# Performance work log

Measured on AMD Instinct MI355X. Metric: run time of the kernel, lower is better.

The kernel has to match this reference:

```python
import jax, jax.numpy as jnp
import numpy as np

B, T, D = 4, 2048, 1024
H, DK, DV = 16, 64, 64


def setup_inputs() -> dict:
    key = jax.random.key(0)
    ks = jax.random.split(key, 12)
    std = 1.0 / np.sqrt(D)
    inp = {
        "query": jax.random.normal(ks[0], (B, T, D), jnp.float32),
        "key": jax.random.normal(ks[1], (B, T, D), jnp.float32),
        "value": jax.random.normal(ks[2], (B, T, D), jnp.float32),
        "mask": jnp.ones((B, 1, 1, T), dtype=bool),
        # weights stored as [in, out] (torch Linear applies x @ W.T + b)
        "Wq": jax.random.truncated_normal(ks[3], -2, 2, (D, H * DK), jnp.float32) * std,
        "bq": jnp.zeros((H * DK,), jnp.float32),
        "Wk": jax.random.truncated_normal(ks[4], -2, 2, (D, H * DK), jnp.float32) * std,
        "bk": jnp.zeros((H * DK,), jnp.float32),
        "Wv": jax.random.truncated_normal(ks[5], -2, 2, (D, H * DV), jnp.float32) * std,
        "bv": jnp.zeros((H * DV,), jnp.float32),
        "Wo": jax.random.truncated_normal(ks[6], -2, 2, (H * DV, D), jnp.float32) * (1.0 / np.sqrt(H * DV)),
        "bo": jnp.zeros((D,), jnp.float32),
    }
    return inp


def reference(query, key, value, mask, Wq, bq, Wk, bk, Wv, bv, Wo, bo):
    denom = 1.0 / np.sqrt(DK)
    q = (query @ Wq + bq).reshape(B, T, H, DK)
    k = (key @ Wk + bk).reshape(B, T, H, DK)
    v = (value @ Wv + bv).reshape(B, T, H, DV)
    # [B, H, T, T] attention logits
    logits = jnp.einsum("bthd,bThd->bhtT", q, k) * denom
    logits = jnp.where(mask, logits, -1e30)
    w = jax.nn.softmax(logits, axis=-1)
    attn = jnp.einsum("bhtT,bThd->bthd", w, v).reshape(B, T, H * DV)
    return attn @ Wo + bo
```

## Files before the change

kernel.cpp:

```cpp
#include <hip/hip_runtime.h>


typedef _Float16 f16;
typedef f16 f16x4 __attribute__((ext_vector_type(4)));
typedef f16 f16x8 __attribute__((ext_vector_type(8)));
typedef __fp16 h16x2 __attribute__((ext_vector_type(2)));
typedef float f32x4 __attribute__((ext_vector_type(4)));

__device__ __forceinline__ void gload_lds16(const void* g, void* l) {
  __builtin_amdgcn_global_load_lds(
      (const __attribute__((address_space(1))) unsigned int*)g,
      (__attribute__((address_space(3))) unsigned int*)l, 16, 0, 0);
}

__device__ __forceinline__ f16x8 cvt8(const f32x4& a, const f32x4& b) {
  h16x2 r0 = __builtin_amdgcn_cvt_pkrtz(a[0], a[1]);
  h16x2 r1 = __builtin_amdgcn_cvt_pkrtz(a[2], a[3]);
  h16x2 r2 = __builtin_amdgcn_cvt_pkrtz(b[0], b[1]);
  h16x2 r3 = __builtin_amdgcn_cvt_pkrtz(b[2], b[3]);
  f16x8 w;
  w[0] = (f16)r0[0]; w[1] = (f16)r0[1]; w[2] = (f16)r1[0]; w[3] = (f16)r1[1];
  w[4] = (f16)r2[0]; w[5] = (f16)r2[1]; w[6] = (f16)r3[0]; w[7] = (f16)r3[1];
  return w;
}

__global__ __launch_bounds__(256) void wtrans(const float* __restrict__ W,
                                              f16* __restrict__ WT) {
  __shared__ float tile[32][33];
  int tx = threadIdx.x, ty = threadIdx.y;
  int o0 = blockIdx.x * 32, i0 = blockIdx.y * 32;
#pragma unroll
  for (int r = 0; r < 32; r += 8)
    tile[ty + r][tx] = W[(size_t)(i0 + ty + r) * 1024 + o0 + tx];
  __syncthreads();
#pragma unroll
  for (int r = 0; r < 32; r += 8)
    WT[(size_t)(o0 + ty + r) * 1024 + i0 + tx] = (f16)tile[tx][ty + r];
}

template <int MODE, bool AF32>
__global__ __launch_bounds__(256) void gemm_bt(const void* __restrict__ Av,
                                               const f16* __restrict__ Bt,
                                               const float* __restrict__ bias,
                                               f16* __restrict__ C16,
                                               float* __restrict__ C32) {
  constexpr int N = 1024, K = 1024;
  constexpr int BM = 128, BN = 128, BK = 32;
  __shared__ f16 As[BM * BK];
  __shared__ f16 Bs[BN * BK];

  const int t = threadIdx.x;
  const int nb = gridDim.x;
  int bid = blockIdx.x;
  int cpx = nb >> 3;
  int swz = (bid & 7) * cpx + (bid >> 3);
  const int ntile = N / BN;
  const int tm = swz / ntile, tn = swz % ntile;

  const int lane = t & 63, w = t >> 6;
  const int wr = w >> 1, wc = w & 1;
  const int lrow = lane & 15, kgrp = lane >> 4;

  f32x4 zero4 = {0.f, 0.f, 0.f, 0.f};
  f32x4 acc[4][4];
#pragma unroll
  for (int mi = 0; mi < 4; ++mi)
#pragma unroll
    for (int ni = 0; ni < 4; ++ni) acc[mi][ni] = zero4;

  const int srow = t >> 2;
  const int scol = (t & 3) * 8;
  const f16* Ag = (const f16*)Av + (size_t)(tm * BM + srow) * K + scol;
  const float* Ag32 = (const float*)Av + (size_t)(tm * BM + srow) * K + scol;
  const f16* Bg = Bt + (size_t)(tn * BN + srow) * K + scol;
  f16* Asl = &As[t * 8];
  f16* Bsl = &Bs[t * 8];

  f32x4 ar[4];
  auto loadA = [&](int k0) {
    ar[0] = *(const f32x4*)(Ag32 + k0);
    ar[1] = *(const f32x4*)(Ag32 + k0 + 4);
    ar[2] = *(const f32x4*)(Ag32 + (size_t)64 * K + k0);
    ar[3] = *(const f32x4*)(Ag32 + (size_t)64 * K + k0 + 4);
  };

  if (AF32) loadA(0);
  for (int k0 = 0; k0 < K; k0 += BK) {
    __syncthreads();
    if (AF32) {
      *(f16x8*)Asl = cvt8(ar[0], ar[1]);
      *(f16x8*)(Asl + 64 * BK) = cvt8(ar[2], ar[3]);
    } else {
      gload_lds16(Ag + k0, Asl);
      gload_lds16(Ag + k0 + (size_t)64 * K, Asl + 64 * BK);
    }
    gload_lds16(Bg + k0, Bsl);
    gload_lds16(Bg + k0 + (size_t)64 * K, Bsl + 64 * BK);
    __syncthreads();
    if (AF32 && k0 + BK < K) loadA(k0 + BK);

    f16x8 af[4], bf[4];
#pragma unroll
    for (int mi = 0; mi < 4; ++mi)
      af[mi] = *(const f16x8*)&As[(wr * 64 + mi * 16 + lrow) * BK + kgrp * 8];
#pragma unroll
    for (int ni = 0; ni < 4; ++ni)
      bf[ni] = *(const f16x8*)&Bs[(wc * 64 + ni * 16 + lrow) * BK + kgrp * 8];
#pragma unroll
    for (int mi = 0; mi < 4; ++mi)
#pragma unroll
      for (int ni = 0; ni < 4; ++ni)
        acc[mi][ni] = __builtin_amdgcn_mfma_f32_16x16x32_f16(af[mi], bf[ni],
                                                             acc[mi][ni], 0, 0, 0);
  }

#pragma unroll
  for (int mi = 0; mi < 4; ++mi) {
#pragma unroll
    for (int ni = 0; ni < 4; ++ni) {
      int col = tn * BN + wc * 64 + ni * 16 + lrow;
      float bv = bias[col];
#pragma unroll
      for (int j = 0; j < 4; ++j) {
        int row = tm * BM + wr * 64 + mi * 16 + kgrp * 4 + j;
        float v = acc[mi][ni][j] + bv;
        if (MODE == 0) {
          C16[(size_t)row * N + col] = (f16)v;
        } else if (MODE == 1) {
          int bb = row >> 11, tt = row & 2047;
          C16[((size_t)(bb * 1024 + col)) * 2048 + tt] = (f16)v;
        } else {
          C32[(size_t)row * N + col] = v;
        }
      }
    }
  }
}

__global__ __launch_bounds__(256) void attn_fwd(const f16* __restrict__ Q,
                                                const f16* __restrict__ Kc,
                                                const f16* __restrict__ Vt,
                                                f16* __restrict__ O) {
  constexpr int T = 2048, HD = 1024, KLD = 88;
  __shared__ f16 Ks[64 * KLD];
  __shared__ f16 Vs[64 * 64];

  const int t = threadIdx.x;
  const int lane = t & 63, w = t >> 6;
  const int lrow = lane & 15, kgrp = lane >> 4;
  int bid = blockIdx.x;
  int swzb = (bid & 7) * 128 + (bid >> 3);
  const int qt = swzb & 15, h = (swzb >> 4) & 15, b = swzb >> 8;

  f16x8 aq[2][2];
#pragma unroll
  for (int g = 0; g < 2; ++g) {
    const f16* qp = Q + (size_t)(b * T + qt * 128 + w * 32 + g * 16 + lrow) * HD +
                    h * 64 + kgrp * 8;
    aq[g][0] = (*(const f16x8*)(qp)) * (f16)0.18033688f;
    aq[g][1] = (*(const f16x8*)(qp + 32)) * (f16)0.18033688f;
  }

  f32x4 zero4 = {0.f, 0.f, 0.f, 0.f};
  float m_r[2] = {-INFINITY, -INFINITY}, l_r[2] = {0.f, 0.f};
  f32x4 oa0[4], oa1[4];
#pragma unroll
  for (int d = 0; d < 4; ++d) { oa0[d] = zero4; oa1[d] = zero4; }

  const int srow = t >> 3;
  const int scol = (t & 7) * 8;
  const int vblk = (t & 7) * 2;
  const int vswz = ((srow & 7) << 1) | ((srow >> 3) & 1);
  const int rswz = ((lrow & 7) << 1) | (lrow >> 3);
  const f16* Kg = Kc + (size_t)(b * T + srow) * HD + h * 64 + scol;
  const f16* Vg = Vt + (size_t)(b * 1024 + h * 64 + srow) * T + scol;

  f16x8 ka0, ka1, va0, va1, kb0, kb1, vb0, vb1;

  auto load_a = [&](int kt) {
    ka0 = *(const f16x8*)(Kg + (size_t)kt * HD);
    ka1 = *(const f16x8*)(Kg + (size_t)(kt + 32) * HD);
    va0 = *(const f16x8*)(Vg + kt);
    va1 = *(const f16x8*)(Vg + kt + 32 * T);
  };
  auto load_b = [&](int kt) {
    kb0 = *(const f16x8*)(Kg + (size_t)kt * HD);
    kb1 = *(const f16x8*)(Kg + (size_t)(kt + 32) * HD);
    vb0 = *(const f16x8*)(Vg + kt);
    vb1 = *(const f16x8*)(Vg + kt + 32 * T);
  };
  auto store_set = [&](f16x8& k0, f16x8& k1, f16x8& v0, f16x8& v1) {
    *(f16x8*)&Ks[srow * KLD + scol] = k0;
    *(f16x8*)&Ks[(srow + 32) * KLD + scol] = k1;
    f16x4* v0h = (f16x4*)&v0;
    f16x4* v1h = (f16x4*)&v1;
    *(f16x4*)&Vs[srow * 64 + ((vblk) ^ vswz) * 4] = v0h[0];
    *(f16x4*)&Vs[srow * 64 + ((vblk + 1) ^ vswz) * 4] = v0h[1];
    *(f16x4*)&Vs[(srow + 32) * 64 + ((vblk) ^ vswz) * 4] = v1h[0];
    *(f16x4*)&Vs[(srow + 32) * 64 + ((vblk + 1) ^ vswz) * 4] = v1h[1];
  };

  auto softmax = [&](f32x4* s, float& mr, float& lr, f32x4* oacc, f16x4* pa) {
    float m0 = fmaxf(fmaxf(s[0][0], s[0][1]), s[0][2]);
    float m1 = fmaxf(fmaxf(s[0][3], s[1][0]), s[1][1]);
    float m2 = fmaxf(fmaxf(s[1][2], s[1][3]), s[2][0]);
    float m3 = fmaxf(fmaxf(s[2][1], s[2][2]), s[2][3]);
    float m4 = fmaxf(fmaxf(s[3][0], s[3][1]), s[3][2]);
    float mx = fmaxf(fmaxf(fmaxf(m0, m1), m2), fmaxf(fmaxf(m3, m4), s[3][3]));
    mx = fmaxf(mx, __shfl_xor(mx, 16, 64));
    mx = fmaxf(mx, __shfl_xor(mx, 32, 64));
    if (__any(mx > mr + 8.f)) {
      float mnew = fmaxf(mr, mx);
      float sc = exp2f(mr - mnew);
      lr *= sc;
      mr = mnew;
#pragma unroll
      for (int d = 0; d < 4; ++d) {
        f32x4 t4 = oacc[d];
        t4[0] *= sc; t4[1] *= sc; t4[2] *= sc; t4[3] *= sc;
        oacc[d] = t4;
      }
    }
    float rs = 0.f;
#pragma unroll
    for (int n = 0; n < 4; ++n) {
      f32x4 p;
#pragma unroll
      for (int j = 0; j < 4; ++j) {
        p[j] = exp2f(s[n][j] - mr);
        rs += p[j];
      }
      h16x2 lo = __builtin_amdgcn_cvt_pkrtz(p[0], p[1]);
      h16x2 hi = __builtin_amdgcn_cvt_pkrtz(p[2], p[3]);
      f16x4 q4;
      q4[0] = (f16)lo[0]; q4[1] = (f16)lo[1];
      q4[2] = (f16)hi[0]; q4[3] = (f16)hi[1];
      pa[n] = q4;
    }
    rs += __shfl_xor(rs, 16, 64);
    rs += __shfl_xor(rs, 32, 64);
    lr += rs;
  };

  auto compute = [&]() {
    f16x8 kf[4][2];
#pragma unroll
    for (int n = 0; n < 4; ++n)
#pragma unroll
      for (int kk = 0; kk < 2; ++kk)
        kf[n][kk] = *(const f16x8*)&Ks[(n * 16 + lrow) * KLD + kk * 32 + kgrp * 8];
    f32x4 s0[4], s1[4];
    __builtin_amdgcn_s_setprio(1);
#pragma unroll
    for (int n = 0; n < 4; ++n) {
      f32x4 a0 = zero4, a1 = zero4;
#pragma unroll
      for (int kk = 0; kk < 2; ++kk) {
        a0 = __builtin_amdgcn_mfma_f32_16x16x32_f16(kf[n][kk], aq[0][kk], a0, 0, 0, 0);
        a1 = __builtin_amdgcn_mfma_f32_16x16x32_f16(kf[n][kk], aq[1][kk], a1, 0, 0, 0);
      }
      s0[n] = a0; s1[n] = a1;
    }
    __builtin_amdgcn_s_setprio(0);

    f16x4 pa0[4], pa1[4];
    softmax(s0, m_r[0], l_r[0], oa0, pa0);
    softmax(s1, m_r[1], l_r[1], oa1, pa1);

    __builtin_amdgcn_s_setprio(1);
#pragma unroll
    for (int d = 0; d < 4; ++d)
#pragma unroll
      for (int n = 0; n < 4; ++n) {
        f16x4 va = *(const f16x4*)&Vs[(d * 16 + lrow) * 64 + ((n * 4 + kgrp) ^ rswz) * 4];
        oa0[d] = __builtin_amdgcn_mfma_f32_16x16x16f16(va, pa0[n], oa0[d], 0, 0, 0);
        oa1[d] = __builtin_amdgcn_mfma_f32_16x16x16f16(va, pa1[n], oa1[d], 0, 0, 0);
      }
    __builtin_amdgcn_s_setprio(0);
  };

  load_a(0);
  for (int kt = 0; kt < T; kt += 128) {
    __syncthreads();
    store_set(ka0, ka1, va0, va1);
    load_b(kt + 64);
    __syncthreads();
    compute();

    __syncthreads();
    store_set(kb0, kb1, vb0, vb1);
    if (kt + 128 < T) load_a(kt + 128);
    __syncthreads();
    compute();
  }

#pragma unroll
  for (int g = 0; g < 2; ++g) {
    float inv = 1.f / l_r[g];
    f32x4* oacc = g ? oa1 : oa0;
    f16* orow = O + (size_t)(b * T + qt * 128 + w * 32 + g * 16 + lrow) * HD + h * 64;
#pragma unroll
    for (int d = 0; d < 4; ++d) {
      f16x4 ov;
      ov[0] = (f16)(oacc[d][0] * inv);
      ov[1] = (f16)(oacc[d][1] * inv);
      ov[2] = (f16)(oacc[d][2] * inv);
      ov[3] = (f16)(oacc[d][3] * inv);
      *(f16x4*)(orow + d * 16 + kgrp * 4) = ov;
    }
  }
}

extern "C" void kernel_launch(void* const* d_in, const int* in_sizes, int n_in,
                              void* d_out, int out_size, void* d_ws, size_t ws_size,
                              hipStream_t stream) {
  (void)in_sizes; (void)n_in; (void)out_size; (void)ws_size;
  const float* query = (const float*)d_in[0];
  const float* key   = (const float*)d_in[1];
  const float* value = (const float*)d_in[2];
  const float* Wq = (const float*)d_in[4];
  const float* bq = (const float*)d_in[5];
  const float* Wk = (const float*)d_in[6];
  const float* bk = (const float*)d_in[7];
  const float* Wv = (const float*)d_in[8];
  const float* bv = (const float*)d_in[9];
  const float* Wo = (const float*)d_in[10];
  const float* bo = (const float*)d_in[11];
  float* out = (float*)d_out;

  f16* ws  = (f16*)d_ws;
  f16* WTq = ws;
  f16* WTk = WTq + 1048576;
  f16* WTv = WTk + 1048576;
  f16* WTo = WTv + 1048576;
  f16* QB  = WTo + 1048576;
  f16* KB  = QB + 8388608;
  f16* VT  = KB + 8388608;
  f16* AB  = VT + 8388608;

  wtrans<<<dim3(32, 32), dim3(32, 8), 0, stream>>>(Wq, WTq);
  wtrans<<<dim3(32, 32), dim3(32, 8), 0, stream>>>(Wk, WTk);
  wtrans<<<dim3(32, 32), dim3(32, 8), 0, stream>>>(Wv, WTv);
  wtrans<<<dim3(32, 32), dim3(32, 8), 0, stream>>>(Wo, WTo);

  gemm_bt<0, true><<<dim3(512), dim3(256), 0, stream>>>(query, WTq, bq, QB, nullptr);
  gemm_bt<0, true><<<dim3(512), dim3(256), 0, stream>>>(key, WTk, bk, KB, nullptr);
  gemm_bt<1, true><<<dim3(512), dim3(256), 0, stream>>>(value, WTv, bv, VT, nullptr);

  attn_fwd<<<dim3(1024), dim3(256), 0, stream>>>(QB, KB, VT, AB);

  gemm_bt<2, false><<<dim3(512), dim3(256), 0, stream>>>(AB, WTo, bo, nullptr, out);
}
```

Baseline: 276.3 us.

## Stream K/V tiles via direct global-to-LDS loads with double buffering and MFMA row sums

The attention kernel now loads K/V tiles with global_load_lds straight into a double-buffered, XOR-swizzled LDS region, instead of staging them through registers and storing them manually. This needs only one barrier per tile instead of two. The softmax row sum moves from VALU adds plus cross-lane shuffles to MFMA against a ones vector, and launch bounds now request 4 blocks per CU. The extra MFMAs and the larger LDS footprint (32KB) may limit occupancy, and the fp16-rounded P values now feed the row sum.

```diff
diff --git a/kernel.cpp b/kernel.cpp
--- a/kernel.cpp
+++ b/kernel.cpp
@@ -137,13 +137,13 @@
   }
 }
 
-__global__ __launch_bounds__(256) void attn_fwd(const f16* __restrict__ Q,
-                                                const f16* __restrict__ Kc,
-                                                const f16* __restrict__ Vt,
-                                                f16* __restrict__ O) {
-  constexpr int T = 2048, HD = 1024, KLD = 88;
-  __shared__ f16 Ks[64 * KLD];
-  __shared__ f16 Vs[64 * 64];
+__global__ __launch_bounds__(256, 4) void attn_fwd(const f16* __restrict__ Q,
+                                                   const f16* __restrict__ Kc,
+                                                   const f16* __restrict__ Vt,
+                                                   f16* __restrict__ O) {
+  constexpr int T = 2048, HD = 1024;
+  __shared__ __align__(16) f16 lds[16384];
+  char* LB = (char*)lds;
 
   const int t = threadIdx.x;
   const int lane = t & 63, w = t >> 6;
@@ -162,58 +162,56 @@
   }
 
   f32x4 zero4 = {0.f, 0.f, 0.f, 0.f};
-  float m_r[2] = {-INFINITY, -INFINITY}, l_r[2] = {0.f, 0.f};
+  float m_r[2] = {-INFINITY, -INFINITY};
   f32x4 oa0[4], oa1[4];
+  f32x4 la0 = zero4, la1 = zero4;
 #pragma unroll
   for (int d = 0; d < 4; ++d) { oa0[d] = zero4; oa1[d] = zero4; }
 
-  const int srow = t >> 3;
-  const int scol = (t & 7) * 8;
-  const int vblk = (t & 7) * 2;
-  const int vswz = ((srow & 7) << 1) | ((srow >> 3) & 1);
-  const int rswz = ((lrow & 7) << 1) | (lrow >> 3);
-  const f16* Kg = Kc + (size_t)(b * T + srow) * HD + h * 64 + scol;
-  const f16* Vg = Vt + (size_t)(b * 1024 + h * 64 + srow) * T + scol;
-
-  f16x8 ka0, ka1, va0, va1, kb0, kb1, vb0, vb1;
-
-  auto load_a = [&](int kt) {
-    ka0 = *(const f16x8*)(Kg + (size_t)kt * HD);
-    ka1 = *(const f16x8*)(Kg + (size_t)(kt + 32) * HD);
-    va0 = *(const f16x8*)(Vg + kt);
-    va1 = *(const f16x8*)(Vg + kt + 32 * T);
+  f16x4 ones;
+  ones[0] = (f16)1.f; ones[1] = (f16)1.f; ones[2] = (f16)1.f; ones[3] = (f16)1.f;
+
+  unsigned kof0 = lrow * 128 + ((kgrp ^ (lrow & 7)) << 4);
+  unsigned kof1 = lrow * 128 + (((4 + kgrp) ^ (lrow & 7)) << 4);
+  unsigned vof[4];
+#pragma unroll
+  for (int n = 0; n < 4; ++n)
+    vof[n] = 8192 + lrow * 128 + (((n * 4 + kgrp) ^ ((lrow & 7) << 1)) << 3);
+
+  unsigned dK0 = w * 2048, dK1 = dK0 + 1024;
+  unsigned dV0 = 8192 + w * 2048, dV1 = dV0 + 1024;
+
+  const int l8 = lane & 7, lr8 = lane >> 3;
+  const int cswz = (l8 ^ lr8) * 8;
+  const int rA = w * 16 + lr8, rB = rA + 8;
+  const f16* kg0 = Kc + (size_t)(b * T + rA) * HD + h * 64 + cswz;
+  const f16* kg1 = Kc + (size_t)(b * T + rB) * HD + h * 64 + cswz;
+  const f16* vg0 = Vt + (size_t)(b * 1024 + h * 64 + rA) * T + cswz;
+  const f16* vg1 = Vt + (size_t)(b * 1024 + h * 64 + rB) * T + cswz;
+
+  auto stage = [&]() {
+    gload_lds16(kg0, LB + dK0);
+    gload_lds16(kg1, LB + dK1);
+    gload_lds16(vg0, LB + dV0);
+    gload_lds16(vg1, LB + dV1);
+    kg0 += (size_t)64 * HD; kg1 += (size_t)64 * HD;
+    vg0 += 64; vg1 += 64;
   };
-  auto load_b = [&](int kt) {
-    kb0 = *(const f16x8*)(Kg + (size_t)kt * HD);
-    kb1 = *(const f16x8*)(Kg + (size_t)(kt + 32) * HD);
-    vb0 = *(const f16x8*)(Vg + kt);
-    vb1 = *(const f16x8*)(Vg + kt + 32 * T);
-  };
-  auto store_set = [&](f16x8& k0, f16x8& k1, f16x8& v0, f16x8& v1) {
-    *(f16x8*)&Ks[srow * KLD + scol] = k0;
-    *(f16x8*)&Ks[(srow + 32) * KLD + scol] = k1;
-    f16x4* v0h = (f16x4*)&v0;
-    f16x4* v1h = (f16x4*)&v1;
-    *(f16x4*)&Vs[srow * 64 + ((vblk) ^ vswz) * 4] = v0h[0];
-    *(f16x4*)&Vs[srow * 64 + ((vblk + 1) ^ vswz) * 4] = v0h[1];
-    *(f16x4*)&Vs[(srow + 32) * 64 + ((vblk) ^ vswz) * 4] = v1h[0];
-    *(f16x4*)&Vs[(srow + 32) * 64 + ((vblk + 1) ^ vswz) * 4] = v1h[1];
-  };
-
-  auto softmax = [&](f32x4* s, float& mr, float& lr, f32x4* oacc, f16x4* pa) {
-    float m0 = fmaxf(fmaxf(s[0][0], s[0][1]), s[0][2]);
-    float m1 = fmaxf(fmaxf(s[0][3], s[1][0]), s[1][1]);
-    float m2 = fmaxf(fmaxf(s[1][2], s[1][3]), s[2][0]);
-    float m3 = fmaxf(fmaxf(s[2][1], s[2][2]), s[2][3]);
-    float m4 = fmaxf(fmaxf(s[3][0], s[3][1]), s[3][2]);
-    float mx = fmaxf(fmaxf(fmaxf(m0, m1), m2), fmaxf(fmaxf(m3, m4), s[3][3]));
+
+  auto softmax = [&](f32x4* s, float& mr, f32x4* oacc, f32x4& lacc, f16x4* pa) {
+    float mx = fmaxf(fmaxf(s[0][0], s[0][1]), s[0][2]);
+    mx = fmaxf(mx, fmaxf(fmaxf(s[0][3], s[1][0]), s[1][1]));
+    mx = fmaxf(mx, fmaxf(fmaxf(s[1][2], s[1][3]), s[2][0]));
+    mx = fmaxf(mx, fmaxf(fmaxf(s[2][1], s[2][2]), s[2][3]));
+    mx = fmaxf(mx, fmaxf(fmaxf(s[3][0], s[3][1]), s[3][2]));
+    mx = fmaxf(mx, s[3][3]);
     mx = fmaxf(mx, __shfl_xor(mx, 16, 64));
     mx = fmaxf(mx, __shfl_xor(mx, 32, 64));
     if (__any(mx > mr + 8.f)) {
       float mnew = fmaxf(mr, mx);
       float sc = exp2f(mr - mnew);
-      lr *= sc;
       mr = mnew;
+      lacc[0] *= sc; lacc[1] *= sc; lacc[2] *= sc; lacc[3] *= sc;
 #pragma unroll
       for (int d = 0; d < 4; ++d) {
         f32x4 t4 = oacc[d];
@@ -221,15 +219,11 @@
         oacc[d] = t4;
       }
     }
-    float rs = 0.f;
 #pragma unroll
     for (int n = 0; n < 4; ++n) {
       f32x4 p;
 #pragma unroll
-      for (int j = 0; j < 4; ++j) {
-        p[j] = exp2f(s[n][j] - mr);
-        rs += p[j];
-      }
+      for (int j = 0; j < 4; ++j) p[j] = exp2f(s[n][j] - mr);
       h16x2 lo = __builtin_amdgcn_cvt_pkrtz(p[0], p[1]);
       h16x2 hi = __builtin_amdgcn_cvt_pkrtz(p[2], p[3]);
       f16x4 q4;
@@ -237,66 +231,67 @@
       q4[2] = (f16)hi[0]; q4[3] = (f16)hi[1];
       pa[n] = q4;
     }
-    rs += __shfl_xor(rs, 16, 64);
-    rs += __shfl_xor(rs, 32, 64);
-    lr += rs;
   };
 
-  auto compute = [&]() {
-    f16x8 kf[4][2];
-#pragma unroll
-    for (int n = 0; n < 4; ++n)
-#pragma unroll
-      for (int kk = 0; kk < 2; ++kk)
-        kf[n][kk] = *(const f16x8*)&Ks[(n * 16 + lrow) * KLD + kk * 32 + kgrp * 8];
+  stage();
+  dK0 ^= 16384; dK1 ^= 16384; dV0 ^= 16384; dV1 ^= 16384;
+  __syncthreads();
+
+  for (int tile = 0; tile < 32; ++tile) {
+    if (tile < 31) stage();
+
+    f16x8 kf0[4], kf1[4];
+#pragma unroll
+    for (int n = 0; n < 4; ++n) {
+      kf0[n] = *(const f16x8*)(LB + (kof0 + n * 2048));
+      kf1[n] = *(const f16x8*)(LB + (kof1 + n * 2048));
+    }
     f32x4 s0[4], s1[4];
     __builtin_amdgcn_s_setprio(1);
 #pragma unroll
     for (int n = 0; n < 4; ++n) {
-      f32x4 a0 = zero4, a1 = zero4;
-#pragma unroll
-      for (int kk = 0; kk < 2; ++kk) {
-        a0 = __builtin_amdgcn_mfma_f32_16x16x32_f16(kf[n][kk], aq[0][kk], a0, 0, 0, 0);
-        a1 = __builtin_amdgcn_mfma_f32_16x16x32_f16(kf[n][kk], aq[1][kk], a1, 0, 0, 0);
-      }
+      f32x4 a0 = __builtin_amdgcn_mfma_f32_16x16x32_f16(kf0[n], aq[0][0], zero4, 0, 0, 0);
+      a0 = __builtin_amdgcn_mfma_f32_16x16x32_f16(kf1[n], aq[0][1], a0, 0, 0, 0);
+      f32x4 a1 = __builtin_amdgcn_mfma_f32_16x16x32_f16(kf0[n], aq[1][0], zero4, 0, 0, 0);
+      a1 = __builtin_amdgcn_mfma_f32_16x16x32_f16(kf1[n], aq[1][1], a1, 0, 0, 0);
       s0[n] = a0; s1[n] = a1;
     }
     __builtin_amdgcn_s_setprio(0);
 
     f16x4 pa0[4], pa1[4];
-    softmax(s0, m_r[0], l_r[0], oa0, pa0);
-    softmax(s1, m_r[1], l_r[1], oa1, pa1);
+    softmax(s0, m_r[0], oa0, la0, pa0);
+    softmax(s1, m_r[1], oa1, la1, pa1);
 
     __builtin_amdgcn_s_setprio(1);
-#pragma unroll
-    for (int d = 0; d < 4; ++d)
+    la0 = __builtin_amdgcn_mfma_f32_16x16x16f16(ones, pa0[0], la0, 0, 0, 0);
+    la0 = __builtin_amdgcn_mfma_f32_16x16x16f16(ones, pa0[1], la0, 0, 0, 0);
+    la0 = __builtin_amdgcn_mfma_f32_16x16x16f16(ones, pa0[2], la0, 0, 0, 0);
+    la0 = __builtin_amdgcn_mfma_f32_16x16x16f16(ones, pa0[3], la0, 0, 0, 0);
+    la1 = __builtin_amdgcn_mfma_f32_16x16x16f16(ones, pa1[0], la1, 0, 0, 0);
+    la1 = __builtin_amdgcn_mfma_f32_16x16x16f16(ones, pa1[1], la1, 0, 0, 0);
+    la1 = __builtin_amdgcn_mfma_f32_16x16x16f16(ones, pa1[2], la1, 0, 0, 0);
+    la1 = __builtin_amdgcn_mfma_f32_16x16x16f16(ones, pa1[3], la1, 0, 0, 0);
+#pragma unroll
+    for (int d = 0; d < 4; ++d) {
 #pragma unroll
       for (int n = 0; n < 4; ++n) {
-        f16x4 va = *(const f16x4*)&Vs[(d * 16 + lrow) * 64 + ((n * 4 + kgrp) ^ rswz) * 4];
+        f16x4 va = *(const f16x4*)(LB + (vof[n] + d * 2048));
         oa0[d] = __builtin_amdgcn_mfma_f32_16x16x16f16(va, pa0[n], oa0[d], 0, 0, 0);
         oa1[d] = __builtin_amdgcn_mfma_f32_16x16x16f16(va, pa1[n], oa1[d], 0, 0, 0);
       }
+    }
     __builtin_amdgcn_s_setprio(0);
-  };
-
-  load_a(0);
-  for (int kt = 0; kt < T; kt += 128) {
+
     __syncthreads();
-    store_set(ka0, ka1, va0, va1);
-    load_b(kt + 64);
-    __syncthreads();
-    compute();
-
-    __syncthreads();
-    store_set(kb0, kb1, vb0, vb1);
-    if (kt + 128 < T) load_a(kt + 128);
-    __syncthreads();
-    compute();
+    kof0 ^= 16384; kof1 ^= 16384;
+#pragma unroll
+    for (int n = 0; n < 4; ++n) vof[n] ^= 16384;
+    dK0 ^= 16384; dK1 ^= 16384; dV0 ^= 16384; dV1 ^= 16384;
   }
 
 #pragma unroll
   for (int g = 0; g < 2; ++g) {
-    float inv = 1.f / l_r[g];
+    float inv = 1.f / (g ? la1[0] : la0[0]);
     f32x4* oacc = g ? oa1 : oa0;
     f16* orow = O + (size_t)(b * T + qt * 128 + w * 32 + g * 16 + lrow) * HD + h * 64;
 #pragma unroll
```

New measurement: 292.9 us. +6.0%, slower.
